# Kernel tuning notes

Measured on AMD Instinct MI355X. Metric: run time of the kernel, lower is better.

Reference implementation:

```python
import jax, jax.numpy as jnp
import numpy as np

VOCAB = 256
UNITS = 512

def setup_inputs() -> dict:
    key = jax.random.key(0)
    ks = jax.random.split(key, 7)
    B, T = 64, 1024
    scale = 0.02
    return {
        "inputs": jax.random.randint(ks[0], (B, T), 0, VOCAB, dtype=jnp.int32),
        "emb": jax.random.normal(ks[1], (VOCAB, VOCAB), dtype=jnp.float32) * scale,
        "Wx": jax.random.normal(ks[2], (VOCAB, UNITS), dtype=jnp.float32) * scale,
        "Wh": jax.random.normal(ks[3], (UNITS, UNITS), dtype=jnp.float32) * scale,
        "b": jnp.zeros((UNITS,), dtype=jnp.float32),
        "Wd": jax.random.normal(ks[4], (UNITS, VOCAB), dtype=jnp.float32) * scale,
        "bd": jnp.zeros((VOCAB,), dtype=jnp.float32),
    }

def reference(inputs, emb, Wx, Wh, b, Wd, bd):
    # Embedding lookup: [B, T] -> [B, T, VOCAB]
    x = emb[inputs]
    B = x.shape[0]
    # Precompute input projection for all timesteps (one big GEMM)
    xp = jnp.einsum("bte,eu->btu", x, Wx) + b  # [B, T, U]
    h0 = jnp.zeros((B, Wh.shape[0]), dtype=x.dtype)

    def step(h, xp_t):
        h_new = jnp.tanh(xp_t + h @ Wh)  # SimpleRNN cell: tanh(x W_x + h W_h + b)
        return h_new, h_new

    _, hs = jax.lax.scan(step, h0, jnp.swapaxes(xp, 0, 1))  # hs: [T, B, U]
    hs = jnp.swapaxes(hs, 0, 1)  # [B, T, U]
    logits = jnp.einsum("btu,uv->btv", hs, Wd) + bd  # [B, T, VOCAB]
    return logits
```

## Files before the change

### kernel.cpp

```cpp
#include <hip/hip_runtime.h>
#include <math.h>

#define BB   64
#define TT_  1024
#define UU   512
#define VV   256
#define EE   256
#define TC   64

__device__ __forceinline__ float tanh_fast(float x) {
    float e = __expf(x + x);
    return 1.f - 2.f * __builtin_amdgcn_rcpf(e + 1.f);
}

__global__ __launch_bounds__(512) void e2_kernel(
    const float* __restrict__ emb, const float* __restrict__ Wx,
    const float* __restrict__ bias, float* __restrict__ E2)
{
    const int v = blockIdx.x;
    const int u = threadIdx.x;
    float acc = bias[u];
    const float* er = emb + v * EE;
    #pragma unroll 8
    for (int e = 0; e < EE; ++e)
        acc = fmaf(er[e], Wx[e * UU + u], acc);
    E2[v * UU + u] = acc;
}

__global__ __launch_bounds__(512, 2) void rnn_chunk_kernel(
    const int* __restrict__ toks, const float* __restrict__ E2,
    const float* __restrict__ Wh, const float* __restrict__ Wd,
    const float* __restrict__ bd,
    unsigned long long* hpub,
    float* out, int t0, int last)
{
    __shared__ float WhLDS[UU * 64];
    __shared__ float hstage[8][2][64];
    __shared__ float partials[2][8][2][64];
    __shared__ float hmine[2][2][64];
    __shared__ int   stok[2][TC];

    const int bid  = blockIdx.x;
    const int bg   = bid & 31;
    const int ug   = bid >> 5;
    const int tid  = threadIdx.x;
    const int w    = tid >> 6;
    const int lane = tid & 63;
    const int u4   = lane & 15;
    const int kq   = lane >> 4;
    const int b0   = bg * 2;

    const float4* Wh4  = (const float4*)Wh;
    float4*       WhL4 = (float4*)WhLDS;
    {
        const int col = tid & 15;
        const int kr0 = tid >> 4;
        #pragma unroll
        for (int p = 0; p < 16; ++p) {
            int k = p * 32 + kr0;
            WhL4[k * 16 + col] = Wh4[k * 128 + ug * 16 + col];
        }
    }
    if (tid < 128) {
        int b = tid >> 6, q = tid & 63;
        stok[b][q] = toks[(b0 + b) * TT_ + t0 + q];
    }
    if (t0 > 0 && tid < 128) {
        int b = tid >> 6, u = tid & 63;
        unsigned long long p =
            hpub[((size_t)((t0 - 1) & 1) * BB + (b0 + b)) * UU + ug * 64 + u];
        hmine[(t0 - 1) & 1][b][u] = __uint_as_float((unsigned int)p);
    }

    const int bmine = w & 1;
    const int vmine = (w >> 1) * 64 + lane;
    float wdreg[64];
    #pragma unroll
    for (int u = 0; u < 64; ++u)
        wdreg[u] = Wd[(ug * 64 + u) * VV + vmine];
    const float bdv = (ug == 0) ? bd[vmine] : 0.f;

    __syncthreads();

    int fails = 0;
    for (int tt = 0; tt < TC; ++tt) {
        const int s = t0 + tt;
        float xp = 0.f;
        if (w < 2) xp = E2[stok[w][tt] * UU + ug * 64 + lane];

        float acc0[4] = {0.f,0.f,0.f,0.f};
        float acc1[4] = {0.f,0.f,0.f,0.f};
        if (s > 0) {
            const int slot = (s - 1) & 1;
            const unsigned int want = (unsigned int)(s - 1);
            unsigned long long* a0 = hpub + ((size_t)slot * BB + b0) * UU + w * 64 + lane;
            unsigned long long* a1 = a0 + UU;
            unsigned long long p0 = 0, p1 = 0;
            bool got = false;
            if (fails < 3) {
                volatile const unsigned long long* f0 = a0;
                volatile const unsigned long long* f1 = a1;
                for (int it = 0; it < 24; ++it) {
                    p0 = *f0; p1 = *f1;
                    unsigned long long ok =
                        __ballot((unsigned int)(p0 >> 32) == want) &
                        __ballot((unsigned int)(p1 >> 32) == want);
                    if (ok == 0xFFFFFFFFFFFFFFFFull) { got = true; break; }
                }
                if (!got) ++fails;
            }
            if (!got) {
                while (true) {
                    p0 = __hip_atomic_load(a0, __ATOMIC_RELAXED, __HIP_MEMORY_SCOPE_AGENT);
                    p1 = __hip_atomic_load(a1, __ATOMIC_RELAXED, __HIP_MEMORY_SCOPE_AGENT);
                    unsigned long long ok =
                        __ballot((unsigned int)(p0 >> 32) == want) &
                        __ballot((unsigned int)(p1 >> 32) == want);
                    if (ok == 0xFFFFFFFFFFFFFFFFull) break;
                    __builtin_amdgcn_s_sleep(1);
                }
            }
            hstage[w][0][lane] = __uint_as_float((unsigned int)p0);
            hstage[w][1][lane] = __uint_as_float((unsigned int)p1);
            const float4* h40 = (const float4*)hstage[w][0];
            const float4* h41 = (const float4*)hstage[w][1];
            #pragma unroll
            for (int r = 0; r < 4; ++r) {
                float4 a = h40[kq * 4 + r];
                float4 c = h41[kq * 4 + r];
                float ha[4] = {a.x, a.y, a.z, a.w};
                float hc[4] = {c.x, c.y, c.z, c.w};
                #pragma unroll
                for (int q = 0; q < 4; ++q) {
                    float4 wv = WhL4[(w * 64 + kq * 16 + r * 4 + q) * 16 + u4];
                    acc0[0] = fmaf(ha[q], wv.x, acc0[0]);
                    acc0[1] = fmaf(ha[q], wv.y, acc0[1]);
                    acc0[2] = fmaf(ha[q], wv.z, acc0[2]);
                    acc0[3] = fmaf(ha[q], wv.w, acc0[3]);
                    acc1[0] = fmaf(hc[q], wv.x, acc1[0]);
                    acc1[1] = fmaf(hc[q], wv.y, acc1[1]);
                    acc1[2] = fmaf(hc[q], wv.z, acc1[2]);
                    acc1[3] = fmaf(hc[q], wv.w, acc1[3]);
                }
            }
        }

        #pragma unroll
        for (int i = 0; i < 4; ++i) {
            acc0[i] += __shfl_xor(acc0[i], 16, 64);
            acc0[i] += __shfl_xor(acc0[i], 32, 64);
            acc1[i] += __shfl_xor(acc1[i], 16, 64);
            acc1[i] += __shfl_xor(acc1[i], 32, 64);
        }
        if (kq == 0) {
            *(float4*)&partials[s & 1][w][0][u4 * 4] =
                make_float4(acc0[0], acc0[1], acc0[2], acc0[3]);
            *(float4*)&partials[s & 1][w][1][u4 * 4] =
                make_float4(acc1[0], acc1[1], acc1[2], acc1[3]);
        }
        __syncthreads();

        if (w < 2) {
            float ssum = xp;
            #pragma unroll
            for (int wv = 0; wv < 8; ++wv)
                ssum += partials[s & 1][wv][w][lane];
            float h = tanh_fast(ssum);
            unsigned long long pk =
                ((unsigned long long)(unsigned int)s << 32) | __float_as_uint(h);
            unsigned long long* dst =
                hpub + ((size_t)(s & 1) * BB + (b0 + w)) * UU + ug * 64 + lane;
            *(volatile unsigned long long*)dst = pk;
            __hip_atomic_store(dst, pk, __ATOMIC_RELAXED, __HIP_MEMORY_SCOPE_AGENT);
            hmine[s & 1][w][lane] = h;
        }

        if (s > 0) {
            const float4* hb = (const float4*)hmine[(s - 1) & 1][bmine];
            float sum = bdv;
            #pragma unroll
            for (int j = 0; j < 16; ++j) {
                float4 h4 = hb[j];
                sum = fmaf(h4.x, wdreg[4*j+0], sum);
                sum = fmaf(h4.y, wdreg[4*j+1], sum);
                sum = fmaf(h4.z, wdreg[4*j+2], sum);
                sum = fmaf(h4.w, wdreg[4*j+3], sum);
            }
            atomicAdd(out + ((size_t)(b0 + bmine) * TT_ + (s - 1)) * VV + vmine, sum);
        }
    }

    if (last) {
        __syncthreads();
        const int s = t0 + TC - 1;
        const float4* hb = (const float4*)hmine[s & 1][bmine];
        float sum = bdv;
        #pragma unroll
        for (int j = 0; j < 16; ++j) {
            float4 h4 = hb[j];
            sum = fmaf(h4.x, wdreg[4*j+0], sum);
            sum = fmaf(h4.y, wdreg[4*j+1], sum);
            sum = fmaf(h4.z, wdreg[4*j+2], sum);
            sum = fmaf(h4.w, wdreg[4*j+3], sum);
        }
        atomicAdd(out + ((size_t)(b0 + bmine) * TT_ + s) * VV + vmine, sum);
    }
}

extern "C" void kernel_launch(void* const* d_in, const int* in_sizes, int n_in,
                              void* d_out, int out_size, void* d_ws, size_t ws_size,
                              hipStream_t stream)
{
    (void)in_sizes; (void)n_in; (void)ws_size;

    const int*   toks = (const int*)  d_in[0];
    const float* emb  = (const float*)d_in[1];
    const float* Wx   = (const float*)d_in[2];
    const float* Wh   = (const float*)d_in[3];
    const float* bias = (const float*)d_in[4];
    const float* Wd   = (const float*)d_in[5];
    const float* bd   = (const float*)d_in[6];
    float* out = (float*)d_out;

    unsigned long long* hpub = (unsigned long long*)d_ws;
    float* E2 = (float*)(hpub + 2 * BB * UU);

    hipMemsetAsync(out, 0, (size_t)out_size * sizeof(float), stream);
    e2_kernel<<<EE, UU, 0, stream>>>(emb, Wx, bias, E2);

    for (int c = 0; c < TT_ / TC; ++c) {
        const int t0 = c * TC;
        rnn_chunk_kernel<<<256, 512, 0, stream>>>(
            toks, E2, Wh, Wd, bd, hpub, out, t0, c == (TT_ / TC - 1));
    }
}
```

Measured before the change: 2.668 ms.

## Hold Wh in registers, split output projection by vocab, drop atomics

Each block now keeps its Wh slice in registers (float4 per lane) instead of LDS. The recurrent dot product is reduced with wave shuffles rather than a cross-wave partials buffer plus an extra barrier. The output projection is repartitioned so each block owns a 32-wide vocab slice over the full hidden vector, which lets logits be written directly instead of atomically accumulated, and removes the output memset. The next step's input projection is prefetched, and the gathered hidden state is staged in swizzled LDS. In exchange every block must now poll all 512 hidden units each step rather than only its own slice, and register pressure rises.

```diff
diff --git a/kernel.cpp b/kernel.cpp
--- a/kernel.cpp
+++ b/kernel.cpp
@@ -34,11 +34,9 @@
     unsigned long long* hpub,
     float* out, int t0, int last)
 {
-    __shared__ float WhLDS[UU * 64];
-    __shared__ float hstage[8][2][64];
-    __shared__ float partials[2][8][2][64];
-    __shared__ float hmine[2][2][64];
-    __shared__ int   stok[2][TC];
+    __shared__ int stok[2][TC];
+    __shared__ __align__(16) float hstage[2][2][UU];
+    __shared__ __align__(16) float xps[2][2][64];
 
     const int bid  = blockIdx.x;
     const int bg   = bid & 31;
@@ -46,68 +44,58 @@
     const int tid  = threadIdx.x;
     const int w    = tid >> 6;
     const int lane = tid & 63;
-    const int u4   = lane & 15;
-    const int kq   = lane >> 4;
     const int b0   = bg * 2;
 
-    const float4* Wh4  = (const float4*)Wh;
-    float4*       WhL4 = (float4*)WhLDS;
+    const int qsel = lane >> 5;
+    const int ks   = lane & 31;
+    const int quad = w * 2 + qsel;
+    const int vloc8 = lane >> 3;
+    const int us8   = lane & 7;
+    const int bL    = w & 1;
+    const int vmine = ug * 32 + (w >> 1) * 8 + vloc8;
+
+    float4 whreg[16];
     {
-        const int col = tid & 15;
-        const int kr0 = tid >> 4;
+        const float4* Wh4 = (const float4*)Wh;
         #pragma unroll
-        for (int p = 0; p < 16; ++p) {
-            int k = p * 32 + kr0;
-            WhL4[k * 16 + col] = Wh4[k * 128 + ug * 16 + col];
-        }
-    }
-    if (tid < 128) {
-        int b = tid >> 6, q = tid & 63;
-        stok[b][q] = toks[(b0 + b) * TT_ + t0 + q];
-    }
-    if (t0 > 0 && tid < 128) {
-        int b = tid >> 6, u = tid & 63;
-        unsigned long long p =
-            hpub[((size_t)((t0 - 1) & 1) * BB + (b0 + b)) * UU + ug * 64 + u];
-        hmine[(t0 - 1) & 1][b][u] = __uint_as_float((unsigned int)p);
-    }
-
-    const int bmine = w & 1;
-    const int vmine = (w >> 1) * 64 + lane;
+        for (int r = 0; r < 16; ++r)
+            whreg[r] = Wh4[(ks * 16 + r) * 128 + ug * 16 + quad];
+    }
     float wdreg[64];
     #pragma unroll
-    for (int u = 0; u < 64; ++u)
-        wdreg[u] = Wd[(ug * 64 + u) * VV + vmine];
-    const float bdv = (ug == 0) ? bd[vmine] : 0.f;
-
+    for (int j = 0; j < 64; ++j)
+        wdreg[j] = Wd[(us8 * 64 + j) * VV + vmine];
+    const float bdv = bd[vmine];
+
+    if (tid < 128) {
+        const int b = tid >> 6, q = tid & 63;
+        stok[b][q] = toks[(b0 + b) * TT_ + t0 + q];
+        xps[0][b][q & 63] = 0.f;
+    }
+    if (tid < 128) {
+        const int b = tid >> 6, u = tid & 63;
+        xps[0][b][u] = E2[toks[(b0 + b) * TT_ + t0] * UU + ug * 64 + u];
+    }
     __syncthreads();
 
-    int fails = 0;
     for (int tt = 0; tt < TC; ++tt) {
-        const int s = t0 + tt;
-        float xp = 0.f;
-        if (w < 2) xp = E2[stok[w][tt] * UU + ug * 64 + lane];
-
-        float acc0[4] = {0.f,0.f,0.f,0.f};
-        float acc1[4] = {0.f,0.f,0.f,0.f};
-        if (s > 0) {
-            const int slot = (s - 1) & 1;
+        const int s  = t0 + tt;
+        const int sl = (s - 1) & 1;
+
+        if (s > 0 && (w != ug || tt == 0)) {
+            unsigned long long* a0 = hpub + ((size_t)sl * BB + b0) * UU + w * 64 + lane;
+            unsigned long long* a1 = a0 + UU;
+            volatile const unsigned long long* f0 = a0;
+            volatile const unsigned long long* f1 = a1;
             const unsigned int want = (unsigned int)(s - 1);
-            unsigned long long* a0 = hpub + ((size_t)slot * BB + b0) * UU + w * 64 + lane;
-            unsigned long long* a1 = a0 + UU;
             unsigned long long p0 = 0, p1 = 0;
             bool got = false;
-            if (fails < 3) {
-                volatile const unsigned long long* f0 = a0;
-                volatile const unsigned long long* f1 = a1;
-                for (int it = 0; it < 24; ++it) {
-                    p0 = *f0; p1 = *f1;
-                    unsigned long long ok =
-                        __ballot((unsigned int)(p0 >> 32) == want) &
-                        __ballot((unsigned int)(p1 >> 32) == want);
-                    if (ok == 0xFFFFFFFFFFFFFFFFull) { got = true; break; }
-                }
-                if (!got) ++fails;
+            for (int it = 0; it < 24; ++it) {
+                p0 = *f0; p1 = *f1;
+                unsigned long long ok =
+                    __ballot((unsigned int)(p0 >> 32) == want) &
+                    __ballot((unsigned int)(p1 >> 32) == want);
+                if (ok == 0xFFFFFFFFFFFFFFFFull) { got = true; break; }
             }
             if (!got) {
                 while (true) {
@@ -120,90 +108,159 @@
                     __builtin_amdgcn_s_sleep(1);
                 }
             }
-            hstage[w][0][lane] = __uint_as_float((unsigned int)p0);
-            hstage[w][1][lane] = __uint_as_float((unsigned int)p1);
-            const float4* h40 = (const float4*)hstage[w][0];
-            const float4* h41 = (const float4*)hstage[w][1];
-            #pragma unroll
-            for (int r = 0; r < 4; ++r) {
-                float4 a = h40[kq * 4 + r];
-                float4 c = h41[kq * 4 + r];
-                float ha[4] = {a.x, a.y, a.z, a.w};
-                float hc[4] = {c.x, c.y, c.z, c.w};
+            const int aa  = w * 16 + (lane >> 2);
+            const int asw = aa ^ ((aa >> 3) & 7);
+            const int fi  = asw * 4 + (lane & 3);
+            hstage[sl][0][fi] = __uint_as_float((unsigned int)p0);
+            hstage[sl][1][fi] = __uint_as_float((unsigned int)p1);
+        }
+        __syncthreads();
+
+        float xpre = 0.f;
+        const bool dopre = (tid < 128) && (tt + 1 < TC);
+        if (dopre)
+            xpre = E2[stok[tid >> 6][tt + 1] * UU + ug * 64 + (tid & 63)];
+
+        float acc0[4] = {0.f, 0.f, 0.f, 0.f};
+        float acc1[4] = {0.f, 0.f, 0.f, 0.f};
+        if (s > 0) {
+            const float* H0 = hstage[sl][0];
+            const float* H1 = hstage[sl][1];
+            const int vsw = (ks >> 1) & 7;
+            #pragma unroll
+            for (int g = 0; g < 4; ++g) {
+                const int as2 = (4 * ks + g) ^ vsw;
+                const float4 ha = *(const float4*)(H0 + as2 * 4);
+                const float4 hc = *(const float4*)(H1 + as2 * 4);
+                const float av[4] = {ha.x, ha.y, ha.z, ha.w};
+                const float cv[4] = {hc.x, hc.y, hc.z, hc.w};
                 #pragma unroll
-                for (int q = 0; q < 4; ++q) {
-                    float4 wv = WhL4[(w * 64 + kq * 16 + r * 4 + q) * 16 + u4];
-                    acc0[0] = fmaf(ha[q], wv.x, acc0[0]);
-                    acc0[1] = fmaf(ha[q], wv.y, acc0[1]);
-                    acc0[2] = fmaf(ha[q], wv.z, acc0[2]);
-                    acc0[3] = fmaf(ha[q], wv.w, acc0[3]);
-                    acc1[0] = fmaf(hc[q], wv.x, acc1[0]);
-                    acc1[1] = fmaf(hc[q], wv.y, acc1[1]);
-                    acc1[2] = fmaf(hc[q], wv.z, acc1[2]);
-                    acc1[3] = fmaf(hc[q], wv.w, acc1[3]);
-                }
-            }
-        }
-
-        #pragma unroll
-        for (int i = 0; i < 4; ++i) {
-            acc0[i] += __shfl_xor(acc0[i], 16, 64);
-            acc0[i] += __shfl_xor(acc0[i], 32, 64);
-            acc1[i] += __shfl_xor(acc1[i], 16, 64);
-            acc1[i] += __shfl_xor(acc1[i], 32, 64);
-        }
-        if (kq == 0) {
-            *(float4*)&partials[s & 1][w][0][u4 * 4] =
-                make_float4(acc0[0], acc0[1], acc0[2], acc0[3]);
-            *(float4*)&partials[s & 1][w][1][u4 * 4] =
-                make_float4(acc1[0], acc1[1], acc1[2], acc1[3]);
+                for (int m = 0; m < 4; ++m) {
+                    const float4 wv = whreg[g * 4 + m];
+                    acc0[0] = fmaf(av[m], wv.x, acc0[0]);
+                    acc0[1] = fmaf(av[m], wv.y, acc0[1]);
+                    acc0[2] = fmaf(av[m], wv.z, acc0[2]);
+                    acc0[3] = fmaf(av[m], wv.w, acc0[3]);
+                    acc1[0] = fmaf(cv[m], wv.x, acc1[0]);
+                    acc1[1] = fmaf(cv[m], wv.y, acc1[1]);
+                    acc1[2] = fmaf(cv[m], wv.z, acc1[2]);
+                    acc1[3] = fmaf(cv[m], wv.w, acc1[3]);
+                }
+            }
+            #pragma unroll
+            for (int off = 1; off < 32; off <<= 1) {
+                #pragma unroll
+                for (int c = 0; c < 4; ++c) {
+                    acc0[c] += __shfl_xor(acc0[c], off, 64);
+                    acc1[c] += __shfl_xor(acc1[c], off, 64);
+                }
+            }
+        }
+        if (dopre)
+            xps[(s + 1) & 1][tid >> 6][tid & 63] = xpre;
+
+        if (ks < 4) {
+            const int c  = ks;
+            const float h0 = tanh_fast(acc0[c] + xps[s & 1][0][quad * 4 + c]);
+            const float h1 = tanh_fast(acc1[c] + xps[s & 1][1][quad * 4 + c]);
+            unsigned long long* dst0 =
+                hpub + ((size_t)(s & 1) * BB + b0) * UU + ug * 64 + quad * 4 + c;
+            unsigned long long* dst1 = dst0 + UU;
+            const unsigned long long tg = (unsigned long long)(unsigned int)s << 32;
+            const unsigned long long pk0 = tg | __float_as_uint(h0);
+            const unsigned long long pk1 = tg | __float_as_uint(h1);
+            *(volatile unsigned long long*)dst0 = pk0;
+            *(volatile unsigned long long*)dst1 = pk1;
+            __hip_atomic_store(dst0, pk0, __ATOMIC_RELAXED, __HIP_MEMORY_SCOPE_AGENT);
+            __hip_atomic_store(dst1, pk1, __ATOMIC_RELAXED, __HIP_MEMORY_SCOPE_AGENT);
+            const int af  = ug * 16 + quad;
+            const int asf = af ^ ((af >> 3) & 7);
+            hstage[s & 1][0][asf * 4 + c] = h0;
+            hstage[s & 1][1][asf * 4 + c] = h1;
+        }
+
+        if (s > 0) {
+            const float* HB = hstage[sl][bL];
+            const int lb  = us8 * 16;
+            const int vlo = (2 * us8) & 7;
+            const int vhi = (2 * us8 + 1) & 7;
+            float l0 = 0.f, l1 = 0.f, l2 = 0.f, l3 = 0.f;
+            #pragma unroll
+            for (int j = 0; j < 16; ++j) {
+                const int as4 = (lb + j) ^ (j < 8 ? vlo : vhi);
+                const float4 h4 = *(const float4*)(HB + as4 * 4);
+                l0 = fmaf(h4.x, wdreg[4 * j + 0], l0);
+                l1 = fmaf(h4.y, wdreg[4 * j + 1], l1);
+                l2 = fmaf(h4.z, wdreg[4 * j + 2], l2);
+                l3 = fmaf(h4.w, wdreg[4 * j + 3], l3);
+            }
+            float sum = (l0 + l1) + (l2 + l3);
+            sum += __shfl_xor(sum, 1, 64);
+            sum += __shfl_xor(sum, 2, 64);
+            sum += __shfl_xor(sum, 4, 64);
+            if (us8 == 0)
+                out[((size_t)(b0 + bL) * TT_ + (s - 1)) * VV + vmine] = sum + bdv;
+        }
+    }
+
+    if (last) {
+        const int s  = t0 + TC - 1;
+        const int sl = s & 1;
+        if (w != ug) {
+            unsigned long long* a0 = hpub + ((size_t)sl * BB + b0) * UU + w * 64 + lane;
+            unsigned long long* a1 = a0 + UU;
+            volatile const unsigned long long* f0 = a0;
+            volatile const unsigned long long* f1 = a1;
+            const unsigned int want = (unsigned int)s;
+            unsigned long long p0 = 0, p1 = 0;
+            bool got = false;
+            for (int it = 0; it < 24; ++it) {
+                p0 = *f0; p1 = *f1;
+                unsigned long long ok =
+                    __ballot((unsigned int)(p0 >> 32) == want) &
+                    __ballot((unsigned int)(p1 >> 32) == want);
+                if (ok == 0xFFFFFFFFFFFFFFFFull) { got = true; break; }
+            }
+            if (!got) {
+                while (true) {
+                    p0 = __hip_atomic_load(a0, __ATOMIC_RELAXED, __HIP_MEMORY_SCOPE_AGENT);
+                    p1 = __hip_atomic_load(a1, __ATOMIC_RELAXED, __HIP_MEMORY_SCOPE_AGENT);
+                    unsigned long long ok =
+                        __ballot((unsigned int)(p0 >> 32) == want) &
+                        __ballot((unsigned int)(p1 >> 32) == want);
+                    if (ok == 0xFFFFFFFFFFFFFFFFull) break;
+                    __builtin_amdgcn_s_sleep(1);
+                }
+            }
+            const int aa  = w * 16 + (lane >> 2);
+            const int asw = aa ^ ((aa >> 3) & 7);
+            const int fi  = asw * 4 + (lane & 3);
+            hstage[sl][0][fi] = __uint_as_float((unsigned int)p0);
+            hstage[sl][1][fi] = __uint_as_float((unsigned int)p1);
         }
         __syncthreads();
-
-        if (w < 2) {
-            float ssum = xp;
-            #pragma unroll
-            for (int wv = 0; wv < 8; ++wv)
-                ssum += partials[s & 1][wv][w][lane];
-            float h = tanh_fast(ssum);
-            unsigned long long pk =
-                ((unsigned long long)(unsigned int)s << 32) | __float_as_uint(h);
-            unsigned long long* dst =
-                hpub + ((size_t)(s & 1) * BB + (b0 + w)) * UU + ug * 64 + lane;
-            *(volatile unsigned long long*)dst = pk;
-            __hip_atomic_store(dst, pk, __ATOMIC_RELAXED, __HIP_MEMORY_SCOPE_AGENT);
-            hmine[s & 1][w][lane] = h;
-        }
-
-        if (s > 0) {
-            const float4* hb = (const float4*)hmine[(s - 1) & 1][bmine];
-            float sum = bdv;
+        {
+            const float* HB = hstage[sl][bL];
+            const int lb  = us8 * 16;
+            const int vlo = (2 * us8) & 7;
+            const int vhi = (2 * us8 + 1) & 7;
+            float l0 = 0.f, l1 = 0.f, l2 = 0.f, l3 = 0.f;
             #pragma unroll
             for (int j = 0; j < 16; ++j) {
-                float4 h4 = hb[j];
-                sum = fmaf(h4.x, wdreg[4*j+0], sum);
-                sum = fmaf(h4.y, wdreg[4*j+1], sum);
-                sum = fmaf(h4.z, wdreg[4*j+2], sum);
-                sum = fmaf(h4.w, wdreg[4*j+3], sum);
-            }
-            atomicAdd(out + ((size_t)(b0 + bmine) * TT_ + (s - 1)) * VV + vmine, sum);
-        }
-    }
-
-    if (last) {
-        __syncthreads();
-        const int s = t0 + TC - 1;
-        const float4* hb = (const float4*)hmine[s & 1][bmine];
-        float sum = bdv;
-        #pragma unroll
-        for (int j = 0; j < 16; ++j) {
-            float4 h4 = hb[j];
-            sum = fmaf(h4.x, wdreg[4*j+0], sum);
-            sum = fmaf(h4.y, wdreg[4*j+1], sum);
-            sum = fmaf(h4.z, wdreg[4*j+2], sum);
-            sum = fmaf(h4.w, wdreg[4*j+3], sum);
-        }
-        atomicAdd(out + ((size_t)(b0 + bmine) * TT_ + s) * VV + vmine, sum);
+                const int as4 = (lb + j) ^ (j < 8 ? vlo : vhi);
+                const float4 h4 = *(const float4*)(HB + as4 * 4);
+                l0 = fmaf(h4.x, wdreg[4 * j + 0], l0);
+                l1 = fmaf(h4.y, wdreg[4 * j + 1], l1);
+                l2 = fmaf(h4.z, wdreg[4 * j + 2], l2);
+                l3 = fmaf(h4.w, wdreg[4 * j + 3], l3);
+            }
+            float sum = (l0 + l1) + (l2 + l3);
+            sum += __shfl_xor(sum, 1, 64);
+            sum += __shfl_xor(sum, 2, 64);
+            sum += __shfl_xor(sum, 4, 64);
+            if (us8 == 0)
+                out[((size_t)(b0 + bL) * TT_ + s) * VV + vmine] = sum + bdv;
+        }
     }
 }
 
@@ -211,7 +268,7 @@
                               void* d_out, int out_size, void* d_ws, size_t ws_size,
                               hipStream_t stream)
 {
-    (void)in_sizes; (void)n_in; (void)ws_size;
+    (void)in_sizes; (void)n_in; (void)ws_size; (void)out_size;
 
     const int*   toks = (const int*)  d_in[0];
     const float* emb  = (const float*)d_in[1];
@@ -225,7 +282,7 @@
     unsigned long long* hpub = (unsigned long long*)d_ws;
     float* E2 = (float*)(hpub + 2 * BB * UU);
 
-    hipMemsetAsync(out, 0, (size_t)out_size * sizeof(float), stream);
+    hipMemsetAsync(hpub, 0xFF, (size_t)(2 * BB * UU) * sizeof(unsigned long long), stream);
     e2_kernel<<<EE, UU, 0, stream>>>(emb, Wx, bias, E2);
 
     for (int c = 0; c < TT_ / TC; ++c) {
```

New measurement: 3.789 ms. 1.42x slower.
